# Optimization experiments

Measured on AMD Instinct MI355X. Metric: run time of the kernel, lower is better.

Reference implementation:

```python
import jax, jax.numpy as jnp
import numpy as np

WS = (5, 3, 1)          # per-level window sizes (CrossLayerPosEmbedding3D default)
STRIDES = (4, 2, 1)
PADS = (2, 1, 0)
HWS = (80, 40, 20)      # per-level map sizes -> 20x20 = 400 windows per level
B, C, NH = 8, 256, 4
HD = C // NH            # head_dim = 64
NTOK = (25, 9, 1)       # tokens per level, total 35
W0 = WS[0]
TABLE = (2 * W0 - 1) ** 2  # 81


def _rel_pos_index():
    # replicates CrossLayerPosEmbedding3D (spatial=True): float cross-scale coords
    coords = []
    for i, w in enumerate(WS):
        c = (np.arange(w) - w // 2).astype(np.float64)
        if i < len(WS) - 1:
            c = c * (W0 / w)
        gh, gw = np.meshgrid(c, c, indexing='ij')
        coords.append(np.stack([gh.reshape(-1), gw.reshape(-1)]))
    cf = np.concatenate(coords, axis=-1)                       # (2, 35)
    rel = (cf[:, :, None] - cf[:, None, :]).transpose(1, 2, 0).copy()
    rel[..., 0] += W0 - 1
    rel[..., 1] += W0 - 1
    rel[..., 0] *= 2 * W0 - 1
    return rel.sum(-1).astype(np.float32)                      # (35, 35) float index

REL_IDX = _rel_pos_index()
LEVEL_OF_TOKEN = np.repeat(np.arange(3), NTOK)                 # (35,)


def unfold(x, k, s, p):
    # torch.nn.functional.unfold -> (B, n_windows, k*k, C) (overlaped_window_partition)
    Bx, Cx, H, W = x.shape
    xp = jnp.pad(x, ((0, 0), (0, 0), (p, p), (p, p)))
    oh = (H + 2 * p - k) // s + 1
    ow = (W + 2 * p - k) // s + 1
    hi = (np.arange(oh) * s)[:, None] + np.arange(k)           # (oh, k)
    wi = (np.arange(ow) * s)[:, None] + np.arange(k)           # (ow, k)
    pt = xp[:, :, hi[:, None, :, None], wi[None, :, None, :]]  # (B, C, oh, ow, k, k)
    return pt.transpose(0, 2, 3, 4, 5, 1).reshape(Bx, oh * ow, k * k, Cx)


def fold(win, H, W, k, s, p):
    # torch.nn.functional.fold (sums overlaps) (overlaped_window_reverse)
    Bx, Wm, _, Cx = win.shape
    oh = (H + 2 * p - k) // s + 1
    ow = (W + 2 * p - k) // s + 1
    Hp, Wp = H + 2 * p, W + 2 * p
    hi = (np.arange(oh) * s)[:, None] + np.arange(k)
    wi = (np.arange(ow) * s)[:, None] + np.arange(k)
    lin = (hi[:, None, :, None] * Wp + wi[None, :, None, :]).reshape(-1)
    vals = win.transpose(0, 3, 1, 2).reshape(Bx, Cx, -1)       # matches (Wm, k*k) flatten order
    canvas = jnp.zeros((Bx, Cx, Hp * Wp), win.dtype).at[:, :, lin].add(vals)
    return canvas.reshape(Bx, Cx, Hp, Wp)[:, :, p:p + H, p:p + W]


def _l2n(x):
    # F.normalize(dim=-1), eps=1e-12
    return x / jnp.maximum(jnp.linalg.norm(x, axis=-1, keepdims=True), 1e-12)


def _forward(x0, x1, x2, w_qkv0, w_qkv1, w_qkv2, w_proj, b_proj, rpb_table, abs_bias):
    xs = (x0, x1, x2)
    wq = (w_qkv0, w_qkv1, w_qkv2)
    qs, ks, vs = [], [], []
    for l in range(3):  # small fixed layer loop (structurally distinct weights)
        t = unfold(xs[l], WS[l], STRIDES[l], PADS[l])          # (B, 400, ws^2, C)
        qkv = jnp.einsum('bwtc,cf->bwtf', t, wq[l])
        Bx, Wm, T, _ = qkv.shape
        qkv = qkv.reshape(Bx, Wm, T, 3, NH, HD).transpose(3, 0, 4, 1, 2, 5)  # (3,B,H,Wm,t,hd)
        qs.append(qkv[0]); ks.append(qkv[1]); vs.append(qkv[2])
    q = jnp.concatenate(qs, axis=-2)                           # (B, H, 400, 35, hd)
    k = jnp.concatenate(ks, axis=-2)
    v = jnp.concatenate(vs, axis=-2)

    # interpolated cross-layer relative position bias (floor/ceil lerp on the table)
    idx = jnp.asarray(REL_IDX.reshape(-1))
    fl = jnp.clip(jnp.floor(idx).astype(jnp.int32), 0, TABLE - 1)
    ce = jnp.clip(jnp.ceil(idx).astype(jnp.int32), 0, TABLE - 1)
    wce = (idx - fl.astype(jnp.float32))[:, None]
    pos = (1.0 - wce) * rpb_table[fl] + wce * rpb_table[ce]    # (1225, NH)
    pos = pos.reshape(sum(NTOK), sum(NTOK), NH).transpose(2, 0, 1)  # (NH, 35, 35)
    # per-level absolute bias added on query-row blocks (torch cat over dim=-2)
    pos = pos + abs_bias[LEVEL_OF_TOKEN].T[:, :, None]

    attn = jnp.einsum('bhwqd,bhwkd->bhwqk', _l2n(q), _l2n(k)) + pos[None, :, None]
    attn = jax.nn.softmax(attn, axis=-1)
    out = jnp.einsum('bhwqk,bhwkd->bhwqd', attn, v)            # (B, H, 400, 35, hd)
    Bx = out.shape[0]
    out = out.transpose(0, 2, 3, 1, 4).reshape(Bx, -1, sum(NTOK), NH * HD)  # (B,400,35,C)
    out = jnp.einsum('bwtc,cf->bwtf', out, w_proj) + b_proj
    outs = jnp.split(out, np.cumsum(NTOK)[:-1].tolist(), axis=2)
    return tuple(fold(o, HWS[l], HWS[l], WS[l], STRIDES[l], PADS[l])
                 for l, o in enumerate(outs))


def setup_inputs() -> dict:
    key = jax.random.key(0)
    ks = jax.random.split(key, 8)
    return {
        'x0': jax.random.normal(ks[0], (B, C, 80, 80), jnp.float32),
        'x1': jax.random.normal(ks[1], (B, C, 40, 40), jnp.float32),
        'x2': jax.random.normal(ks[2], (B, C, 20, 20), jnp.float32),
        'w_qkv0': jax.random.normal(ks[3], (C, 3 * C), jnp.float32) * 0.02,
        'w_qkv1': jax.random.normal(ks[4], (C, 3 * C), jnp.float32) * 0.02,
        'w_qkv2': jax.random.normal(ks[5], (C, 3 * C), jnp.float32) * 0.02,
        'w_proj': jax.random.normal(ks[6], (C, C), jnp.float32) * 0.02,
        'b_proj': jnp.zeros((C,), jnp.float32),
        'rpb_table': jax.random.normal(ks[7], (TABLE, NH), jnp.float32) * 0.02,
        'abs_bias': jnp.zeros((3, NH), jnp.float32),
    }


def reference(x0, x1, x2, w_qkv0, w_qkv1, w_qkv2, w_proj, b_proj, rpb_table, abs_bias):
    return _forward(x0, x1, x2, w_qkv0, w_qkv1, w_qkv2, w_proj, b_proj, rpb_table, abs_bias)
```

## Files before the change

kernel.cpp:

```cpp
#include <hip/hip_runtime.h>
#include <math.h>

namespace {

typedef _Float16 half8v __attribute__((ext_vector_type(8)));
typedef _Float16 half4v __attribute__((ext_vector_type(4)));
typedef float    floatx4 __attribute__((ext_vector_type(4)));

constexpr int B   = 8;
constexpr int C   = 256;
constexpr int NH  = 4;
constexpr int HD  = 64;
constexpr int NWIN = 400;
constexpr int NT  = 35;
constexpr int QKVN = 768;
constexpr int RPB = NWIN * NT;

constexpr size_t QKV_B  = (size_t)8400 * QKVN * 2;
constexpr size_t OATT_B = (size_t)RPB * C * 2;
constexpr size_t YT_B   = (size_t)RPB * C * 4;
constexpr size_t PB_B   = QKV_B + OATT_B + YT_B;
constexpr size_t WT_B   = (size_t)3 * QKVN * C * 2;
constexpr size_t POS_B  = 19712;

__device__ inline void token_coord(int j, double& cy, double& cx) {
  if (j < 25)      { int ty = j / 5,  tx = j % 5;  cy = (double)(ty - 2); cx = (double)(tx - 2); }
  else if (j < 34) { int t = j - 25; int ty = t / 3, tx = t % 3;
                     cy = (double)(ty - 1) * (5.0 / 3.0); cx = (double)(tx - 1) * (5.0 / 3.0); }
  else             { cy = 0.0; cx = 0.0; }
}

__global__ void pos_kernel(const float* __restrict__ rpb, const float* __restrict__ ab,
                           float* __restrict__ pos) {
  int p = blockIdx.x * blockDim.x + threadIdx.x;
  if (p >= NH * NT * NT) return;
  int j = p % NT, i = (p / NT) % NT, h = p / (NT * NT);
  double cyi, cxi, cyj, cxj;
  token_coord(i, cyi, cxi);
  token_coord(j, cyj, cxj);
  float fidx = (float)(((cyi - cyj) + 4.0) * 9.0 + ((cxi - cxj) + 4.0));
  int fl = min(max((int)floorf(fidx), 0), 80);
  int ce = min(max((int)ceilf(fidx), 0), 80);
  float w = fidx - (float)fl;
  float pv = (1.0f - w) * rpb[fl * NH + h] + w * rpb[ce * NH + h];
  int li = (i < 25) ? 0 : ((i < 34) ? 1 : 2);
  pos[p] = pv + ab[li * NH + h];
}

__global__ __launch_bounds__(256) void wt_kernel(const float* __restrict__ w0,
                                                 const float* __restrict__ w1,
                                                 const float* __restrict__ w2,
                                                 _Float16* __restrict__ wt) {
  const int bx = blockIdx.x;
  const float* src = bx < 12 ? w0 : (bx < 24 ? w1 : w2);
  _Float16* dst = wt + (size_t)(bx / 12) * QKVN * C;
  const int m0 = (bx % 12) * 64;
  __shared__ _Float16 t[64][264];
  const int tid = threadIdx.x;
  const int p4 = (tid & 15) * 4;
#pragma unroll
  for (int it = 0; it < 16; ++it) {
    int c = it * 16 + (tid >> 4);
    floatx4 v = *(const floatx4*)(src + (size_t)c * QKVN + m0 + p4);
#pragma unroll
    for (int i = 0; i < 4; ++i) t[p4 + i][c] = (_Float16)v[i];
  }
  __syncthreads();
#pragma unroll
  for (int e0 = 0; e0 < 8; ++e0) {
    int e = e0 * 256 + tid;
    int p = e >> 5, c8 = e & 31;
    *(half8v*)(dst + (size_t)(m0 + p) * C + c8 * 8) = *(const half8v*)&t[p][c8 * 8];
  }
}

__global__ __launch_bounds__(256) void qkv_gemm(const float* __restrict__ X0,
                                                const float* __restrict__ X1,
                                                const float* __restrict__ X2,
                                                const _Float16* __restrict__ Wt,
                                                _Float16* __restrict__ Y0,
                                                _Float16* __restrict__ Y1,
                                                _Float16* __restrict__ Y2,
                                                int mb0, int mb01, int g) {
  __shared__ _Float16 As[64][264];
  __shared__ _Float16 Bs[2][128][40];

  int mblk = blockIdx.y;
  const int ny = blockIdx.x;
  const float* X; const _Float16* WtL; _Float16* Y; int HW;
  if (mblk < mb0)       { X = X0; WtL = Wt;                 Y = Y0; HW = 6400; }
  else if (mblk < mb01) { X = X1; WtL = Wt + QKVN * C;      Y = Y1; HW = 1600; mblk -= mb0; }
  else                  { X = X2; WtL = Wt + 2 * QKVN * C;  Y = Y2; HW =  400; mblk -= mb01; }
  const int Mg = g * HW;

  const int tid  = threadIdx.x;
  const int m0   = mblk * 64;
  const int w    = tid >> 6;
  const int lane = tid & 63;
  const int quad = lane >> 4;
  const int mn   = lane & 15;

  {
    const int r  = tid & 63;
    const int ob = tid >> 6;
    int gm = min(m0 + r, Mg - 1);
    int bb = gm / HW, pix = gm - bb * HW;
    const float* xb = X + (size_t)bb * C * HW + pix;
#pragma unroll
    for (int i = 0; i < 8; ++i) {
      int oct = ob + 4 * i;
      const float* xp = xb + (size_t)oct * 8 * HW;
      half8v hv;
#pragma unroll
      for (int j = 0; j < 8; ++j) hv[j] = (_Float16)xp[(size_t)j * HW];
      *(half8v*)&As[r][oct * 8] = hv;
    }
  }

  int rr[2], k8[2];
#pragma unroll
  for (int u = 0; u < 2; ++u) { int e = u * 256 + tid; rr[u] = e >> 2; k8[u] = e & 3; }

  const int nt0 = ny * 3;
  half8v bpre[2];
  auto PLOAD = [&](int st) {
    int nt = nt0 + (st >> 3);
    int k0 = (st & 7) * 32;
#pragma unroll
    for (int u = 0; u < 2; ++u)
      bpre[u] = *(const half8v*)(WtL + (size_t)(nt * 128 + rr[u]) * C + k8[u] * 8 + k0);
  };

  PLOAD(0);
#pragma unroll
  for (int u = 0; u < 2; ++u) *(half8v*)&Bs[0][rr[u]][k8[u] * 8] = bpre[u];
  PLOAD(1);
  __syncthreads();

  int cur = 0;
  for (int nt = nt0; nt < nt0 + 3; ++nt) {
    floatx4 acc[8] = {};
    for (int k0 = 0; k0 < C; k0 += 32) {
#pragma unroll
      for (int u = 0; u < 2; ++u) *(half8v*)&Bs[cur ^ 1][rr[u]][k8[u] * 8] = bpre[u];
      int st2 = (nt - nt0) * 8 + (k0 >> 5) + 2;
      if (st2 < 24) PLOAD(st2);
      half8v a0 = *(const half8v*)&As[w * 16 + mn][k0 + quad * 8];
#pragma unroll
      for (int ni = 0; ni < 8; ++ni) {
        half8v bf = *(const half8v*)&Bs[cur][ni * 16 + mn][quad * 8];
        acc[ni] = __builtin_amdgcn_mfma_f32_16x16x32_f16(a0, bf, acc[ni], 0, 0, 0);
      }
      cur ^= 1;
      __syncthreads();
    }

    const int n0 = nt * 128;
    const bool do_norm = (n0 < 512);
#pragma unroll
    for (int r = 0; r < 4; ++r) {
      float s0 = 0.f, s1 = 0.f;
#pragma unroll
      for (int ni = 0; ni < 4; ++ni) { float vv = acc[ni][r]; s0 += vv * vv; }
#pragma unroll
      for (int ni = 4; ni < 8; ++ni) { float vv = acc[ni][r]; s1 += vv * vv; }
      s0 += __shfl_xor(s0, 1); s1 += __shfl_xor(s1, 1);
      s0 += __shfl_xor(s0, 2); s1 += __shfl_xor(s1, 2);
      s0 += __shfl_xor(s0, 4); s1 += __shfl_xor(s1, 4);
      s0 += __shfl_xor(s0, 8); s1 += __shfl_xor(s1, 8);
      float sc0 = do_norm ? (1.f / fmaxf(sqrtf(s0), 1e-12f)) : 1.f;
      float sc1 = do_norm ? (1.f / fmaxf(sqrtf(s1), 1e-12f)) : 1.f;
      int row = m0 + w * 16 + quad * 4 + r;
      if (row < Mg) {
#pragma unroll
        for (int ni = 0; ni < 8; ++ni)
          Y[(size_t)row * QKVN + n0 + ni * 16 + mn] =
              (_Float16)(acc[ni][r] * (ni < 4 ? sc0 : sc1));
      }
    }
  }
}

__device__ inline const _Float16* token_row_ptr(int j, int wy, int wx, int b,
                                                const _Float16* q0, const _Float16* q1,
                                                const _Float16* q2) {
  if (j >= NT) return nullptr;
  int k_, s_, p_, Hl, t; const _Float16* base;
  if (j < 25)      { k_ = 5; s_ = 4; p_ = 2; Hl = 80; t = j;      base = q0; }
  else if (j < 34) { k_ = 3; s_ = 2; p_ = 1; Hl = 40; t = j - 25; base = q1; }
  else             { k_ = 1; s_ = 1; p_ = 0; Hl = 20; t = 0;      base = q2; }
  int ty = t / k_, tx = t % k_;
  int y = wy * s_ + ty - p_;
  int x = wx * s_ + tx - p_;
  if ((unsigned)y >= (unsigned)Hl || (unsigned)x >= (unsigned)Hl) return nullptr;
  return base + ((size_t)b * Hl * Hl + (size_t)y * Hl + x) * QKVN;
}

__global__ __launch_bounds__(256, 4) void attn_kernel(const _Float16* __restrict__ qkv0,
                                                      const _Float16* __restrict__ qkv1,
                                                      const _Float16* __restrict__ qkv2,
                                                      const float* __restrict__ pos,
                                                      _Float16* __restrict__ O) {
  const int blk = blockIdx.x;
  const int w   = blk % NWIN;
  const int b   = blk / NWIN;
  const int wy = w / 20, wx = w % 20;
  const int tid  = threadIdx.x;
  const int h    = tid >> 6;
  const int lane = tid & 63;
  const int i16  = lane & 15;
  const int q4   = lane >> 4;

  __shared__ __align__(16) _Float16 vrows[48][260];

#pragma unroll
  for (int e0 = 0; e0 < 1536; e0 += 256) {
    int e = e0 + tid;
    int j = e >> 5, cc = e & 31;
    half8v val = (half8v)(_Float16)0.f;
    if (j < NT) {
      const _Float16* rp = token_row_ptr(j, wy, wx, b, qkv0, qkv1, qkv2);
      if (rp) val = *(const half8v*)(rp + 512 + cc * 8);
    }
    *(half8v*)&vrows[j][cc * 8] = val;
  }

  half8v qf[3][2], kf[3][2];
#pragma unroll
  for (int t = 0; t < 3; ++t) {
    const _Float16* rp = token_row_ptr(t * 16 + i16, wy, wx, b, qkv0, qkv1, qkv2);
#pragma unroll
    for (int kc = 0; kc < 2; ++kc) {
      if (rp) {
        qf[t][kc] = *(const half8v*)(rp + h * HD + kc * 32 + q4 * 8);
        kf[t][kc] = *(const half8v*)(rp + 256 + h * HD + kc * 32 + q4 * 8);
      } else {
        qf[t][kc] = (half8v)(_Float16)0.f;
        kf[t][kc] = (half8v)(_Float16)0.f;
      }
    }
  }

  floatx4 s[3][3] = {};
#pragma unroll
  for (int kc = 0; kc < 2; ++kc)
#pragma unroll
    for (int tj = 0; tj < 3; ++tj)
#pragma unroll
      for (int ti = 0; ti < 3; ++ti)
        s[tj][ti] = __builtin_amdgcn_mfma_f32_16x16x32_f16(kf[tj][kc], qf[ti][kc], s[tj][ti], 0, 0, 0);

#pragma unroll
  for (int tj = 0; tj < 3; ++tj)
#pragma unroll
    for (int ti = 0; ti < 3; ++ti)
#pragma unroll
      for (int r = 0; r < 4; ++r) {
        int j = tj * 16 + q4 * 4 + r;
        int i = ti * 16 + i16;
        if (j < NT) { if (i < NT) s[tj][ti][r] += pos[(h * NT + i) * NT + j]; }
        else s[tj][ti][r] = -INFINITY;
      }

  half4v pa[3][3];
#pragma unroll
  for (int ti = 0; ti < 3; ++ti) {
    float m = s[0][ti][0];
#pragma unroll
    for (int tj = 0; tj < 3; ++tj)
#pragma unroll
      for (int r = 0; r < 4; ++r) m = fmaxf(m, s[tj][ti][r]);
    m = fmaxf(m, __shfl_xor(m, 16));
    m = fmaxf(m, __shfl_xor(m, 32));
    float sum = 0.f;
#pragma unroll
    for (int tj = 0; tj < 3; ++tj)
#pragma unroll
      for (int r = 0; r < 4; ++r) { float e = expf(s[tj][ti][r] - m); s[tj][ti][r] = e; sum += e; }
    sum += __shfl_xor(sum, 16);
    sum += __shfl_xor(sum, 32);
    float inv = 1.f / sum;
#pragma unroll
    for (int tj = 0; tj < 3; ++tj)
#pragma unroll
      for (int r = 0; r < 4; ++r) pa[tj][ti][r] = (_Float16)(s[tj][ti][r] * inv);
  }

  __syncthreads();

  half4v vb[3][4];
#pragma unroll
  for (int tj = 0; tj < 3; ++tj)
#pragma unroll
    for (int n = 0; n < 4; ++n)
#pragma unroll
      for (int kk = 0; kk < 4; ++kk)
        vb[tj][n][kk] = vrows[tj * 16 + q4 * 4 + kk][h * HD + n * 16 + i16];

  const size_t obase = ((size_t)(b * NWIN + w) * NT) * C + h * HD;
#pragma unroll
  for (int ti = 0; ti < 3; ++ti) {
    floatx4 o[4] = {};
#pragma unroll
    for (int tj = 0; tj < 3; ++tj)
#pragma unroll
      for (int n = 0; n < 4; ++n)
        o[n] = __builtin_amdgcn_mfma_f32_16x16x16f16(pa[tj][ti], vb[tj][n], o[n], 0, 0, 0);
#pragma unroll
    for (int r = 0; r < 4; ++r) {
      int i = ti * 16 + q4 * 4 + r;
      if (i < NT) {
#pragma unroll
        for (int n = 0; n < 4; ++n)
          O[obase + (size_t)i * C + n * 16 + i16] = (_Float16)o[n][r];
      }
    }
  }
}

__global__ __launch_bounds__(256) void proj_gemm(const _Float16* __restrict__ A,
                                                 const float* __restrict__ W,
                                                 const float* __restrict__ bias,
                                                 float* __restrict__ Yt, int Mg) {
  __shared__ __align__(16) char smem[128 * 69 * 4];
  _Float16 (*As)[40] = (_Float16(*)[40])smem;
  _Float16 (*Bs)[40] = (_Float16(*)[40])(smem + 128 * 40 * 2);
  float    (*Cs)[69] = (float(*)[69])smem;

  const int tid  = threadIdx.x;
  const int m0   = blockIdx.x * 128;
  const int n0   = blockIdx.y * 64;
  const int w    = tid >> 6;
  const int lane = tid & 63;
  const int quad = lane >> 4;
  const int mn   = lane & 15;

  int aM[2], aK8[2], aRow[2];
#pragma unroll
  for (int u = 0; u < 2; ++u) {
    int e = u * 256 + tid;
    aM[u] = e >> 2; aK8[u] = e & 3;
    aRow[u] = min(m0 + aM[u], Mg - 1);
  }

  half8v apre[2]; float bpre[8];
  auto PLOAD = [&](int k0) {
#pragma unroll
    for (int u = 0; u < 2; ++u)
      apre[u] = *(const half8v*)&A[(size_t)aRow[u] * C + k0 + 8 * aK8[u]];
    const float* wp = W + (size_t)(k0 + w * 8) * C + n0 + lane;
#pragma unroll
    for (int j = 0; j < 8; ++j) bpre[j] = wp[(size_t)j * C];
  };

  PLOAD(0);
  floatx4 acc[2][4] = {};
  for (int k0 = 0; k0 < C; k0 += 32) {
#pragma unroll
    for (int u = 0; u < 2; ++u) *(half8v*)&As[aM[u]][8 * aK8[u]] = apre[u];
    {
      half8v hv;
#pragma unroll
      for (int j = 0; j < 8; ++j) hv[j] = (_Float16)bpre[j];
      *(half8v*)&Bs[lane][w * 8] = hv;
    }
    __syncthreads();
    if (k0 + 32 < C) PLOAD(k0 + 32);
    half8v a0 = *(const half8v*)&As[w * 32 + mn][quad * 8];
    half8v a1 = *(const half8v*)&As[w * 32 + 16 + mn][quad * 8];
#pragma unroll
    for (int ni = 0; ni < 4; ++ni) {
      half8v bf = *(const half8v*)&Bs[ni * 16 + mn][quad * 8];
      acc[0][ni] = __builtin_amdgcn_mfma_f32_16x16x32_f16(a0, bf, acc[0][ni], 0, 0, 0);
      acc[1][ni] = __builtin_amdgcn_mfma_f32_16x16x32_f16(a1, bf, acc[1][ni], 0, 0, 0);
    }
    __syncthreads();
  }

#pragma unroll
  for (int mi = 0; mi < 2; ++mi)
#pragma unroll
    for (int r = 0; r < 4; ++r)
#pragma unroll
      for (int ni = 0; ni < 4; ++ni)
        Cs[w * 32 + mi * 16 + quad * 4 + r][ni * 16 + mn] =
            acc[mi][ni][r] + bias[n0 + ni * 16 + mn];
  __syncthreads();
#pragma unroll
  for (int u = 0; u < 32; ++u) {
    int e = u * 256 + tid;
    int ml = e & 127, cl = e >> 7;
    int m = m0 + ml;
    if (m < Mg) {
      int bb = m / RPB;
      int r = m - bb * RPB;
      Yt[((size_t)bb * C + n0 + cl) * RPB + r] = Cs[ml][cl];
    }
  }
}

__global__ __launch_bounds__(256) void fold_kernel(const float* __restrict__ Yt,
                                                   float* __restrict__ out,
                                                   int k_, int s_, int p_, int H_,
                                                   int toff, int total) {
  int idx = blockIdx.x * 256 + threadIdx.x;
  if (idx >= total) return;
  int x = idx % H_;
  int y = (idx / H_) % H_;
  int c = (idx / (H_ * H_)) % C;
  int b = idx / (C * H_ * H_);
  int py = y + p_, px = x + p_;
  int ay = py - k_ + 1;
  int wy_lo = ay <= 0 ? 0 : (ay + s_ - 1) / s_;
  int wy_hi = min(19, py / s_);
  int ax = px - k_ + 1;
  int wx_lo = ax <= 0 ? 0 : (ax + s_ - 1) / s_;
  int wx_hi = min(19, px / s_);
  const float* base = Yt + ((size_t)b * C + c) * RPB;
  float acc = 0.f;
  for (int wy = wy_lo; wy <= wy_hi; ++wy) {
    int tyy = py - wy * s_;
    for (int wx = wx_lo; wx <= wx_hi; ++wx) {
      int txx = px - wx * s_;
      acc += base[(wy * 20 + wx) * NT + toff + tyy * k_ + txx];
    }
  }
  out[idx] = acc;
}

}

extern "C" void kernel_launch(void* const* d_in, const int* in_sizes, int n_in,
                              void* d_out, int out_size, void* d_ws, size_t ws_size,
                              hipStream_t stream) {
  const float* x0    = (const float*)d_in[0];
  const float* x1    = (const float*)d_in[1];
  const float* x2    = (const float*)d_in[2];
  const float* wq0   = (const float*)d_in[3];
  const float* wq1   = (const float*)d_in[4];
  const float* wq2   = (const float*)d_in[5];
  const float* wproj = (const float*)d_in[6];
  const float* bproj = (const float*)d_in[7];
  const float* rpb   = (const float*)d_in[8];
  const float* ab    = (const float*)d_in[9];
  float* out = (float*)d_out;

  int g = 8;
  while (g > 1 && POS_B + (size_t)g * PB_B + WT_B > ws_size) g >>= 1;

  char* ws = (char*)d_ws;
  float*    posb  = (float*)ws;
  _Float16* qkv0g = (_Float16*)(ws + POS_B);
  _Float16* qkv1g = qkv0g + (size_t)g * 6400 * QKVN;
  _Float16* qkv2g = qkv1g + (size_t)g * 1600 * QKVN;
  _Float16* oatt  = qkv2g + (size_t)g *  400 * QKVN;
  float*    yt    = (float*)(ws + POS_B + (size_t)g * (QKV_B + OATT_B));
  _Float16* wt    = (_Float16*)(ws + POS_B + (size_t)g * PB_B);

  pos_kernel<<<(NH * NT * NT + 255) / 256, 256, 0, stream>>>(rpb, ab, posb);
  wt_kernel<<<36, 256, 0, stream>>>(wq0, wq1, wq2, wt);

  const size_t off1 = (size_t)B * C * 6400;
  const size_t off2 = off1 + (size_t)B * C * 1600;

  const int mb0 = (g * 6400 + 63) / 64;
  const int mb1 = (g * 1600 + 63) / 64;
  const int mb2 = (g *  400 + 63) / 64;

  for (int b0 = 0; b0 < B; b0 += g) {
    const float* x0g = x0 + (size_t)b0 * C * 6400;
    const float* x1g = x1 + (size_t)b0 * C * 1600;
    const float* x2g = x2 + (size_t)b0 * C * 400;

    qkv_gemm<<<dim3(2, mb0 + mb1 + mb2), 256, 0, stream>>>(
        x0g, x1g, x2g, wt, qkv0g, qkv1g, qkv2g, mb0, mb0 + mb1, g);

    attn_kernel<<<g * NWIN, 256, 0, stream>>>(qkv0g, qkv1g, qkv2g, posb, oatt);

    proj_gemm<<<dim3((g * RPB + 127) / 128, C / 64), 256, 0, stream>>>(oatt, wproj, bproj, yt, g * RPB);

    const int tot0 = g * C * 6400;
    const int tot1 = g * C * 1600;
    const int tot2 = g * C * 400;
    fold_kernel<<<(tot0 + 255) / 256, 256, 0, stream>>>(yt, out + (size_t)b0 * C * 6400,        5, 4, 2, 80, 0,  tot0);
    fold_kernel<<<(tot1 + 255) / 256, 256, 0, stream>>>(yt, out + off1 + (size_t)b0 * C * 1600, 3, 2, 1, 40, 25, tot1);
    fold_kernel<<<(tot2 + 255) / 256, 256, 0, stream>>>(yt, out + off2 + (size_t)b0 * C * 400,  1, 1, 0, 20, 34, tot2);
  }
}
```

Measured before the change: 468.6 us.

## Alias QKV and projection buffers, single-buffer weight tile, fuse fold launches

The workspace layout now places the QKV buffers and the projection output (yt) at the same address, since QKV is dead by the time proj_gemm writes yt. This shrinks per-group memory so a larger batch group g fits in the workspace. The qkv_gemm weight tile drops from double to single buffering, adding a barrier per k-step, and the weight prefetch is issued before the activation load. The three per-level fold launches are merged into one kernel that branches on the index range. The main risk is aliasing: oatt is placed after yt and must not overlap the QKV data that attn_kernel reads.

```diff
diff --git a/kernel.cpp b/kernel.cpp
--- a/kernel.cpp
+++ b/kernel.cpp
@@ -19,7 +19,7 @@
 constexpr size_t QKV_B  = (size_t)8400 * QKVN * 2;
 constexpr size_t OATT_B = (size_t)RPB * C * 2;
 constexpr size_t YT_B   = (size_t)RPB * C * 4;
-constexpr size_t PB_B   = QKV_B + OATT_B + YT_B;
+constexpr size_t PBA_B  = YT_B + OATT_B;
 constexpr size_t WT_B   = (size_t)3 * QKVN * C * 2;
 constexpr size_t POS_B  = 19712;
 
@@ -83,7 +83,7 @@
                                                 _Float16* __restrict__ Y2,
                                                 int mb0, int mb01, int g) {
   __shared__ _Float16 As[64][264];
-  __shared__ _Float16 Bs[2][128][40];
+  __shared__ _Float16 Bs[128][40];
 
   int mblk = blockIdx.y;
   const int ny = blockIdx.x;
@@ -100,6 +100,22 @@
   const int quad = lane >> 4;
   const int mn   = lane & 15;
 
+  int rr[2], k8[2];
+#pragma unroll
+  for (int u = 0; u < 2; ++u) { int e = u * 256 + tid; rr[u] = e >> 2; k8[u] = e & 3; }
+
+  const int nt0 = ny * 3;
+  half8v bpre[2];
+  auto PLOAD = [&](int st) {
+    int nt = nt0 + (st >> 3);
+    int k0 = (st & 7) * 32;
+#pragma unroll
+    for (int u = 0; u < 2; ++u)
+      bpre[u] = *(const half8v*)(WtL + (size_t)(nt * 128 + rr[u]) * C + k8[u] * 8 + k0);
+  };
+
+  PLOAD(0);
+
   {
     const int r  = tid & 63;
     const int ob = tid >> 6;
@@ -117,45 +133,26 @@
     }
   }
 
-  int rr[2], k8[2];
-#pragma unroll
-  for (int u = 0; u < 2; ++u) { int e = u * 256 + tid; rr[u] = e >> 2; k8[u] = e & 3; }
-
-  const int nt0 = ny * 3;
-  half8v bpre[2];
-  auto PLOAD = [&](int st) {
-    int nt = nt0 + (st >> 3);
-    int k0 = (st & 7) * 32;
-#pragma unroll
-    for (int u = 0; u < 2; ++u)
-      bpre[u] = *(const half8v*)(WtL + (size_t)(nt * 128 + rr[u]) * C + k8[u] * 8 + k0);
-  };
-
-  PLOAD(0);
-#pragma unroll
-  for (int u = 0; u < 2; ++u) *(half8v*)&Bs[0][rr[u]][k8[u] * 8] = bpre[u];
-  PLOAD(1);
-  __syncthreads();
-
-  int cur = 0;
-  for (int nt = nt0; nt < nt0 + 3; ++nt) {
+  for (int ntl = 0; ntl < 3; ++ntl) {
     floatx4 acc[8] = {};
-    for (int k0 = 0; k0 < C; k0 += 32) {
-#pragma unroll
-      for (int u = 0; u < 2; ++u) *(half8v*)&Bs[cur ^ 1][rr[u]][k8[u] * 8] = bpre[u];
-      int st2 = (nt - nt0) * 8 + (k0 >> 5) + 2;
-      if (st2 < 24) PLOAD(st2);
+#pragma unroll
+    for (int kk = 0; kk < 8; ++kk) {
+#pragma unroll
+      for (int u = 0; u < 2; ++u) *(half8v*)&Bs[rr[u]][k8[u] * 8] = bpre[u];
+      __syncthreads();
+      int pst = ntl * 8 + kk + 1;
+      if (pst < 24) PLOAD(pst);
+      const int k0 = kk * 32;
       half8v a0 = *(const half8v*)&As[w * 16 + mn][k0 + quad * 8];
 #pragma unroll
       for (int ni = 0; ni < 8; ++ni) {
-        half8v bf = *(const half8v*)&Bs[cur][ni * 16 + mn][quad * 8];
+        half8v bf = *(const half8v*)&Bs[ni * 16 + mn][quad * 8];
         acc[ni] = __builtin_amdgcn_mfma_f32_16x16x32_f16(a0, bf, acc[ni], 0, 0, 0);
       }
-      cur ^= 1;
       __syncthreads();
     }
 
-    const int n0 = nt * 128;
+    const int n0 = (nt0 + ntl) * 128;
     const bool do_norm = (n0 < 512);
 #pragma unroll
     for (int r = 0; r < 4; ++r) {
@@ -399,16 +396,27 @@
   }
 }
 
-__global__ __launch_bounds__(256) void fold_kernel(const float* __restrict__ Yt,
-                                                   float* __restrict__ out,
-                                                   int k_, int s_, int p_, int H_,
-                                                   int toff, int total) {
+__global__ __launch_bounds__(256) void fold_all(const float* __restrict__ Yt,
+                                                float* __restrict__ out, int b0,
+                                                int tot0, int tot01, int tot012) {
   int idx = blockIdx.x * 256 + threadIdx.x;
-  if (idx >= total) return;
-  int x = idx % H_;
-  int y = (idx / H_) % H_;
-  int c = (idx / (H_ * H_)) % C;
-  int b = idx / (C * H_ * H_);
+  if (idx >= tot012) return;
+  int k_, s_, p_, H_, toff, local;
+  float* dst;
+  if (idx < tot0) {
+    k_ = 5; s_ = 4; p_ = 2; H_ = 80; toff = 0;  local = idx;
+    dst = out + (size_t)b0 * C * 6400;
+  } else if (idx < tot01) {
+    k_ = 3; s_ = 2; p_ = 1; H_ = 40; toff = 25; local = idx - tot0;
+    dst = out + (size_t)B * C * 6400 + (size_t)b0 * C * 1600;
+  } else {
+    k_ = 1; s_ = 1; p_ = 0; H_ = 20; toff = 34; local = idx - tot01;
+    dst = out + (size_t)B * C * (6400 + 1600) + (size_t)b0 * C * 400;
+  }
+  int x = local % H_;
+  int y = (local / H_) % H_;
+  int c = (local / (H_ * H_)) % C;
+  int b = local / (C * H_ * H_);
   int py = y + p_, px = x + p_;
   int ay = py - k_ + 1;
   int wy_lo = ay <= 0 ? 0 : (ay + s_ - 1) / s_;
@@ -425,7 +433,7 @@
       acc += base[(wy * 20 + wx) * NT + toff + tyy * k_ + txx];
     }
   }
-  out[idx] = acc;
+  dst[local] = acc;
 }
 
 }
@@ -446,22 +454,20 @@
   float* out = (float*)d_out;
 
   int g = 8;
-  while (g > 1 && POS_B + (size_t)g * PB_B + WT_B > ws_size) g >>= 1;
+  while (g > 1 && POS_B + WT_B + (size_t)g * PBA_B > ws_size) g >>= 1;
 
   char* ws = (char*)d_ws;
   float*    posb  = (float*)ws;
-  _Float16* qkv0g = (_Float16*)(ws + POS_B);
+  _Float16* wt    = (_Float16*)(ws + POS_B);
+  char*     base  = ws + POS_B + WT_B;
+  _Float16* qkv0g = (_Float16*)base;
   _Float16* qkv1g = qkv0g + (size_t)g * 6400 * QKVN;
   _Float16* qkv2g = qkv1g + (size_t)g * 1600 * QKVN;
-  _Float16* oatt  = qkv2g + (size_t)g *  400 * QKVN;
-  float*    yt    = (float*)(ws + POS_B + (size_t)g * (QKV_B + OATT_B));
-  _Float16* wt    = (_Float16*)(ws + POS_B + (size_t)g * PB_B);
+  float*    yt    = (float*)base;
+  _Float16* oatt  = (_Float16*)(base + (size_t)g * YT_B);
 
   pos_kernel<<<(NH * NT * NT + 255) / 256, 256, 0, stream>>>(rpb, ab, posb);
   wt_kernel<<<36, 256, 0, stream>>>(wq0, wq1, wq2, wt);
-
-  const size_t off1 = (size_t)B * C * 6400;
-  const size_t off2 = off1 + (size_t)B * C * 1600;
 
   const int mb0 = (g * 6400 + 63) / 64;
   const int mb1 = (g * 1600 + 63) / 64;
@@ -479,11 +485,9 @@
 
     proj_gemm<<<dim3((g * RPB + 127) / 128, C / 64), 256, 0, stream>>>(oatt, wproj, bproj, yt, g * RPB);
 
-    const int tot0 = g * C * 6400;
-    const int tot1 = g * C * 1600;
-    const int tot2 = g * C * 400;
-    fold_kernel<<<(tot0 + 255) / 256, 256, 0, stream>>>(yt, out + (size_t)b0 * C * 6400,        5, 4, 2, 80, 0,  tot0);
-    fold_kernel<<<(tot1 + 255) / 256, 256, 0, stream>>>(yt, out + off1 + (size_t)b0 * C * 1600, 3, 2, 1, 40, 25, tot1);
-    fold_kernel<<<(tot2 + 255) / 256, 256, 0, stream>>>(yt, out + off2 + (size_t)b0 * C * 400,  1, 1, 0, 20, 34, tot2);
-  }
-}
+    const int tot0  = g * C * 6400;
+    const int tot01 = tot0 + g * C * 1600;
+    const int tot012 = tot01 + g * C * 400;
+    fold_all<<<(tot012 + 255) / 256, 256, 0, stream>>>(yt, out, b0, tot0, tot01, tot012);
+  }
+}
```

Result: faster. 409.3 us (-12.6%).
